# Optimization experiments

Measured on AMD Instinct MI355X. Metric: run time of the kernel, lower is better.

## Reference

```python
import jax, jax.numpy as jnp
import numpy as np

K = 512  # number of activations kept per row (init_kwargs k)


def setup_inputs() -> dict:
    key = jax.random.key(0)
    x = jax.random.normal(key, (8192, 8192), dtype=jnp.float32)
    return {"x": x}


def reference(x):
    # torch.topk(x, k, dim=1) -> indices of k largest per row
    _, idx = jax.lax.top_k(x, K)                      # idx: [B, K]
    rows = jnp.arange(x.shape[0])[:, None]            # [B, 1]
    # zeros_like + scatter(1, idx, 1)
    mask = jnp.zeros_like(x).at[rows, idx].set(1.0)   # [B, F]
    return x * mask
```

## Files before the change

kernel.cpp:

```cpp
#include <hip/hip_runtime.h>
#include <stdint.h>

#define FDIM 8192
#define KSEL 512
#define NT   512
#define EPT  (FDIM / NT / 4)
#define NBIN 4096
#define NWAVE (NT / 64)

__device__ __forceinline__ unsigned keyOf(unsigned u) {
    return (u & 0x80000000u) ? ~u : (u | 0x80000000u);
}
__device__ __forceinline__ float valOf(unsigned key) {
    unsigned u = (key & 0x80000000u) ? (key ^ 0x80000000u) : ~key;
    return __uint_as_float(u);
}

__global__ __launch_bounds__(NT) void topk_mask_kernel(const float* __restrict__ x,
                                                       float* __restrict__ out) {
    __shared__ uint4 hist4[NBIN / 4];
    unsigned* hist = (unsigned*)hist4;
    __shared__ unsigned wtot[NWAVE];
    __shared__ unsigned s_prefix, s_need, s_sub, s_tiecnt;
    __shared__ unsigned tiebuf[64];

    const int row  = blockIdx.x;
    const int t    = threadIdx.x;
    const int lane = t & 63;
    const int wave = t >> 6;

    const float4* xrow = (const float4*)(x + (size_t)row * FDIM);
    float4*       orow = (float4*)(out + (size_t)row * FDIM);

    uint4 kreg[EPT];
    #pragma unroll
    for (int j = 0; j < EPT; ++j) {
        float4 v = xrow[j * NT + t];
        kreg[j].x = keyOf(__float_as_uint(v.x));
        kreg[j].y = keyOf(__float_as_uint(v.y));
        kreg[j].z = keyOf(__float_as_uint(v.z));
        kreg[j].w = keyOf(__float_as_uint(v.w));
    }
    #pragma unroll
    for (int i = t; i < NBIN / 4; i += NT) hist4[i] = make_uint4(0u, 0u, 0u, 0u);
    if (t == 0) { s_prefix = 0u; s_need = KSEL; s_tiecnt = 0u; }
    __syncthreads();

    #pragma unroll
    for (int round = 0; round < 3; ++round) {
        const unsigned pref = s_prefix;
        const unsigned need = s_need;

        if (round == 0) {
            #pragma unroll
            for (int j = 0; j < EPT; ++j) {
                #pragma unroll
                for (int c = 0; c < 4; ++c) {
                    unsigned key = (&kreg[j].x)[c];
                    atomicAdd(&hist[key >> 20], 1u);
                }
            }
        } else if (round == 1) {
            #pragma unroll
            for (int j = 0; j < EPT; ++j) {
                #pragma unroll
                for (int c = 0; c < 4; ++c) {
                    unsigned key = (&kreg[j].x)[c];
                    if ((key >> 20) == pref)
                        atomicAdd(&hist[(key >> 8) & 0xFFFu], 1u);
                }
            }
        } else {
            #pragma unroll
            for (int j = 0; j < EPT; ++j) {
                #pragma unroll
                for (int c = 0; c < 4; ++c) {
                    unsigned key = (&kreg[j].x)[c];
                    if ((key >> 8) == pref)
                        atomicAdd(&hist[key & 0xFFu], 1u);
                }
            }
        }
        __syncthreads();

        const unsigned b4 = (unsigned)t * 2u;
        const uint4 h0 = hist4[b4];
        const uint4 h1 = hist4[b4 + 1];
        unsigned sfx[9];
        sfx[8] = 0u;
        sfx[7] = h1.w;
        sfx[6] = sfx[7] + h1.z;
        sfx[5] = sfx[6] + h1.y;
        sfx[4] = sfx[5] + h1.x;
        sfx[3] = sfx[4] + h0.w;
        sfx[2] = sfx[3] + h0.z;
        sfx[1] = sfx[2] + h0.y;
        sfx[0] = sfx[1] + h0.x;
        hist4[b4]     = make_uint4(0u, 0u, 0u, 0u);
        hist4[b4 + 1] = make_uint4(0u, 0u, 0u, 0u);
        const unsigned tot = sfx[0];
        unsigned incl = tot;
        #pragma unroll
        for (int off = 1; off < 64; off <<= 1) {
            unsigned y = __shfl_down(incl, off);
            incl += (lane + off < 64) ? y : 0u;
        }
        if (lane == 0) wtot[wave] = incl;
        __syncthreads();
        unsigned gb = incl - tot;
        #pragma unroll
        for (int w = 0; w < NWAVE; ++w) gb += (w > wave) ? wtot[w] : 0u;

        const unsigned base = (unsigned)t * (NBIN / NT);
        #pragma unroll
        for (int i = 0; i < 8; ++i) {
            unsigned S = gb + sfx[i];
            unsigned h = sfx[i] - sfx[i + 1];
            if (S >= need && S - h < need) {
                s_prefix = (round == 2) ? ((pref << 8) | (base + (unsigned)i))
                                        : ((pref << 12) | (base + (unsigned)i));
                s_need = need - (S - h);
                s_sub  = h;
            }
        }
        __syncthreads();
    }

    const unsigned thresh = s_prefix;
    const unsigned keepEq = s_need;
    const unsigned eqCnt  = s_sub;
    const bool simple = (eqCnt == keepEq);

    if (simple) {
        #pragma unroll
        for (int j = 0; j < EPT; ++j) {
            uint4 k = kreg[j];
            float4 o;
            o.x = (k.x >= thresh) ? valOf(k.x) : 0.0f;
            o.y = (k.y >= thresh) ? valOf(k.y) : 0.0f;
            o.z = (k.z >= thresh) ? valOf(k.z) : 0.0f;
            o.w = (k.w >= thresh) ? valOf(k.w) : 0.0f;
            orow[j * NT + t] = o;
        }
    } else {
        #pragma unroll
        for (int j = 0; j < EPT; ++j) {
            uint4 k = kreg[j];
            float4 o;
            o.x = (k.x > thresh) ? valOf(k.x) : 0.0f;
            o.y = (k.y > thresh) ? valOf(k.y) : 0.0f;
            o.z = (k.z > thresh) ? valOf(k.z) : 0.0f;
            o.w = (k.w > thresh) ? valOf(k.w) : 0.0f;
            orow[j * NT + t] = o;
        }
        #pragma unroll
        for (int j = 0; j < EPT; ++j) {
            #pragma unroll
            for (int c = 0; c < 4; ++c) {
                unsigned key = (&kreg[j].x)[c];
                if (key == thresh) {
                    unsigned slot = atomicAdd(&s_tiecnt, 1u);
                    if (slot < 64u) tiebuf[slot] = 4u * (unsigned)(j * NT + t) + (unsigned)c;
                }
            }
        }
        __syncthreads();
        if (t == 0) {
            const unsigned m = s_tiecnt;
            const float v = valOf(thresh);
            if (m <= 64u) {
                for (unsigned i = 0; i < m; ++i) {
                    unsigned idx = tiebuf[i], rank = 0;
                    for (unsigned q = 0; q < m; ++q) rank += (tiebuf[q] < idx);
                    if (rank < keepEq) out[(size_t)row * FDIM + idx] = v;
                }
            } else {
                unsigned c = 0;
                for (int i = 0; i < FDIM && c < keepEq; ++i) {
                    if (keyOf(__float_as_uint(x[(size_t)row * FDIM + i])) == thresh) {
                        out[(size_t)row * FDIM + i] = v; ++c;
                    }
                }
            }
        }
    }
}

extern "C" void kernel_launch(void* const* d_in, const int* in_sizes, int n_in,
                              void* d_out, int out_size, void* d_ws, size_t ws_size,
                              hipStream_t stream) {
    const float* x = (const float*)d_in[0];
    float* out = (float*)d_out;
    topk_mask_kernel<<<dim3(FDIM), dim3(NT), 0, stream>>>(x, out);
}
```

Before: 439.2 us.

## Make kernel persistent over rows with register double-buffered prefetch of next row

Launches 1024 blocks that each process 8 rows, prefetching the next row's data into a second register buffer while the current row's radix-select runs, so global load latency overlaps the histogram work. Barriers are replaced with custom waitcnt and s_barrier sequences that wait only on LDS so the outstanding prefetch loads are not drained, and keyOf becomes branchless. This doubles the per-thread register footprint for row data, and launch_bounds(NT,4) may force spills or limit occupancy.

```diff
diff --git a/kernel.cpp b/kernel.cpp
--- a/kernel.cpp
+++ b/kernel.cpp
@@ -7,56 +7,70 @@
 #define EPT  (FDIM / NT / 4)
 #define NBIN 4096
 #define NWAVE (NT / 64)
+#define NBLK 1024
+#define RPB  (FDIM / NBLK)
 
 __device__ __forceinline__ unsigned keyOf(unsigned u) {
-    return (u & 0x80000000u) ? ~u : (u | 0x80000000u);
+    return u ^ ((unsigned)((int)u >> 31) | 0x80000000u);
 }
 __device__ __forceinline__ float valOf(unsigned key) {
     unsigned u = (key & 0x80000000u) ? (key ^ 0x80000000u) : ~key;
     return __uint_as_float(u);
 }
 
-__global__ __launch_bounds__(NT) void topk_mask_kernel(const float* __restrict__ x,
-                                                       float* __restrict__ out) {
-    __shared__ uint4 hist4[NBIN / 4];
-    unsigned* hist = (unsigned*)hist4;
-    __shared__ unsigned wtot[NWAVE];
-    __shared__ unsigned s_prefix, s_need, s_sub, s_tiecnt;
-    __shared__ unsigned tiebuf[64];
-
-    const int row  = blockIdx.x;
-    const int t    = threadIdx.x;
-    const int lane = t & 63;
-    const int wave = t >> 6;
-
-    const float4* xrow = (const float4*)(x + (size_t)row * FDIM);
-    float4*       orow = (float4*)(out + (size_t)row * FDIM);
-
-    uint4 kreg[EPT];
+__device__ __forceinline__ void barrier_lgkm() {
+    asm volatile("s_waitcnt lgkmcnt(0)" ::: "memory");
+    __builtin_amdgcn_s_barrier();
+}
+__device__ __forceinline__ void barrier_full() {
+    asm volatile("s_waitcnt vmcnt(0) lgkmcnt(0)" ::: "memory");
+    __builtin_amdgcn_s_barrier();
+}
+
+struct Shared {
+    uint4 hist4[NBIN / 4];
+    unsigned wtot[NWAVE];
+    unsigned s_prefix, s_need;
+    unsigned s_thresh, s_keepEq, s_eqCnt;
+    unsigned s_tiecnt;
+    unsigned tiebuf[64];
+};
+
+__device__ __forceinline__ void process_row(
+    const int row, const bool doPrefetch, const int nextRow,
+    const float* __restrict__ x, float* __restrict__ out,
+    uint4 (&cur)[EPT], uint4 (&nxt)[EPT],
+    Shared& sh, const int t, const int lane, const int wave)
+{
+    if (doPrefetch) {
+        const uint4* xr = (const uint4*)(x + (size_t)nextRow * FDIM);
+        #pragma unroll
+        for (int j = 0; j < EPT; ++j) nxt[j] = xr[j * NT + t];
+    }
+
     #pragma unroll
     for (int j = 0; j < EPT; ++j) {
-        float4 v = xrow[j * NT + t];
-        kreg[j].x = keyOf(__float_as_uint(v.x));
-        kreg[j].y = keyOf(__float_as_uint(v.y));
-        kreg[j].z = keyOf(__float_as_uint(v.z));
-        kreg[j].w = keyOf(__float_as_uint(v.w));
-    }
-    #pragma unroll
-    for (int i = t; i < NBIN / 4; i += NT) hist4[i] = make_uint4(0u, 0u, 0u, 0u);
-    if (t == 0) { s_prefix = 0u; s_need = KSEL; s_tiecnt = 0u; }
-    __syncthreads();
+        cur[j].x = keyOf(cur[j].x);
+        cur[j].y = keyOf(cur[j].y);
+        cur[j].z = keyOf(cur[j].z);
+        cur[j].w = keyOf(cur[j].w);
+    }
+    if (t == 0) { sh.s_prefix = 0u; sh.s_need = KSEL; sh.s_tiecnt = 0u; }
+    barrier_lgkm();
+
+    unsigned* hist = (unsigned*)sh.hist4;
 
     #pragma unroll
     for (int round = 0; round < 3; ++round) {
-        const unsigned pref = s_prefix;
-        const unsigned need = s_need;
+        const unsigned pref = sh.s_prefix;
+        const unsigned need = sh.s_need;
 
         if (round == 0) {
             #pragma unroll
             for (int j = 0; j < EPT; ++j) {
                 #pragma unroll
                 for (int c = 0; c < 4; ++c) {
-                    unsigned key = (&kreg[j].x)[c];
+                    unsigned key = (&cur[j].x)[c];
                     atomicAdd(&hist[key >> 20], 1u);
                 }
             }
@@ -65,7 +79,7 @@
             for (int j = 0; j < EPT; ++j) {
                 #pragma unroll
                 for (int c = 0; c < 4; ++c) {
-                    unsigned key = (&kreg[j].x)[c];
+                    unsigned key = (&cur[j].x)[c];
                     if ((key >> 20) == pref)
                         atomicAdd(&hist[(key >> 8) & 0xFFFu], 1u);
                 }
@@ -75,17 +89,17 @@
             for (int j = 0; j < EPT; ++j) {
                 #pragma unroll
                 for (int c = 0; c < 4; ++c) {
-                    unsigned key = (&kreg[j].x)[c];
+                    unsigned key = (&cur[j].x)[c];
                     if ((key >> 8) == pref)
                         atomicAdd(&hist[key & 0xFFu], 1u);
                 }
             }
         }
-        __syncthreads();
+        barrier_lgkm();
 
         const unsigned b4 = (unsigned)t * 2u;
-        const uint4 h0 = hist4[b4];
-        const uint4 h1 = hist4[b4 + 1];
+        const uint4 h0 = sh.hist4[b4];
+        const uint4 h1 = sh.hist4[b4 + 1];
         unsigned sfx[9];
         sfx[8] = 0u;
         sfx[7] = h1.w;
@@ -96,8 +110,8 @@
         sfx[2] = sfx[3] + h0.z;
         sfx[1] = sfx[2] + h0.y;
         sfx[0] = sfx[1] + h0.x;
-        hist4[b4]     = make_uint4(0u, 0u, 0u, 0u);
-        hist4[b4 + 1] = make_uint4(0u, 0u, 0u, 0u);
+        sh.hist4[b4]     = make_uint4(0u, 0u, 0u, 0u);
+        sh.hist4[b4 + 1] = make_uint4(0u, 0u, 0u, 0u);
         const unsigned tot = sfx[0];
         unsigned incl = tot;
         #pragma unroll
@@ -105,11 +119,12 @@
             unsigned y = __shfl_down(incl, off);
             incl += (lane + off < 64) ? y : 0u;
         }
-        if (lane == 0) wtot[wave] = incl;
-        __syncthreads();
+        if (lane == 0) sh.wtot[wave] = incl;
+        barrier_lgkm();
+
         unsigned gb = incl - tot;
         #pragma unroll
-        for (int w = 0; w < NWAVE; ++w) gb += (w > wave) ? wtot[w] : 0u;
+        for (int w = 0; w < NWAVE; ++w) gb += (w > wave) ? sh.wtot[w] : 0u;
 
         const unsigned base = (unsigned)t * (NBIN / NT);
         #pragma unroll
@@ -117,24 +132,30 @@
             unsigned S = gb + sfx[i];
             unsigned h = sfx[i] - sfx[i + 1];
             if (S >= need && S - h < need) {
-                s_prefix = (round == 2) ? ((pref << 8) | (base + (unsigned)i))
-                                        : ((pref << 12) | (base + (unsigned)i));
-                s_need = need - (S - h);
-                s_sub  = h;
-            }
-        }
-        __syncthreads();
-    }
-
-    const unsigned thresh = s_prefix;
-    const unsigned keepEq = s_need;
-    const unsigned eqCnt  = s_sub;
+                if (round == 2) {
+                    sh.s_thresh = (pref << 8) | (base + (unsigned)i);
+                    sh.s_keepEq = need - (S - h);
+                    sh.s_eqCnt  = h;
+                } else {
+                    sh.s_prefix = (pref << 12) | (base + (unsigned)i);
+                    sh.s_need   = need - (S - h);
+                }
+            }
+        }
+        barrier_lgkm();
+    }
+
+    const unsigned thresh = sh.s_thresh;
+    const unsigned keepEq = sh.s_keepEq;
+    const unsigned eqCnt  = sh.s_eqCnt;
     const bool simple = (eqCnt == keepEq);
 
+    float4* orow = (float4*)(out + (size_t)row * FDIM);
+
     if (simple) {
         #pragma unroll
         for (int j = 0; j < EPT; ++j) {
-            uint4 k = kreg[j];
+            uint4 k = cur[j];
             float4 o;
             o.x = (k.x >= thresh) ? valOf(k.x) : 0.0f;
             o.y = (k.y >= thresh) ? valOf(k.y) : 0.0f;
@@ -145,7 +166,7 @@
     } else {
         #pragma unroll
         for (int j = 0; j < EPT; ++j) {
-            uint4 k = kreg[j];
+            uint4 k = cur[j];
             float4 o;
             o.x = (k.x > thresh) ? valOf(k.x) : 0.0f;
             o.y = (k.y > thresh) ? valOf(k.y) : 0.0f;
@@ -157,21 +178,21 @@
         for (int j = 0; j < EPT; ++j) {
             #pragma unroll
             for (int c = 0; c < 4; ++c) {
-                unsigned key = (&kreg[j].x)[c];
+                unsigned key = (&cur[j].x)[c];
                 if (key == thresh) {
-                    unsigned slot = atomicAdd(&s_tiecnt, 1u);
-                    if (slot < 64u) tiebuf[slot] = 4u * (unsigned)(j * NT + t) + (unsigned)c;
-                }
-            }
-        }
-        __syncthreads();
+                    unsigned slot = atomicAdd(&sh.s_tiecnt, 1u);
+                    if (slot < 64u) sh.tiebuf[slot] = 4u * (unsigned)(j * NT + t) + (unsigned)c;
+                }
+            }
+        }
+        barrier_full();
         if (t == 0) {
-            const unsigned m = s_tiecnt;
+            const unsigned m = sh.s_tiecnt;
             const float v = valOf(thresh);
             if (m <= 64u) {
                 for (unsigned i = 0; i < m; ++i) {
-                    unsigned idx = tiebuf[i], rank = 0;
-                    for (unsigned q = 0; q < m; ++q) rank += (tiebuf[q] < idx);
+                    unsigned idx = sh.tiebuf[i], rank = 0;
+                    for (unsigned q = 0; q < m; ++q) rank += (sh.tiebuf[q] < idx);
                     if (rank < keepEq) out[(size_t)row * FDIM + idx] = v;
                 }
             } else {
@@ -186,10 +207,37 @@
     }
 }
 
+__global__ __launch_bounds__(NT, 4) void topk_mask_kernel(const float* __restrict__ x,
+                                                          float* __restrict__ out) {
+    __shared__ Shared sh;
+
+    const int blk  = blockIdx.x;
+    const int t    = threadIdx.x;
+    const int lane = t & 63;
+    const int wave = t >> 6;
+
+    uint4 rawA[EPT], rawB[EPT];
+    {
+        const uint4* xr = (const uint4*)(x + (size_t)blk * FDIM);
+        #pragma unroll
+        for (int j = 0; j < EPT; ++j) rawA[j] = xr[j * NT + t];
+    }
+    #pragma unroll
+    for (int i = t; i < NBIN / 4; i += NT) sh.hist4[i] = make_uint4(0u, 0u, 0u, 0u);
+
+    #pragma unroll 1
+    for (int r = 0; r < RPB; r += 2) {
+        process_row(r * NBLK + blk, true, (r + 1) * NBLK + blk,
+                    x, out, rawA, rawB, sh, t, lane, wave);
+        process_row((r + 1) * NBLK + blk, (r + 2) < RPB, (r + 2) * NBLK + blk,
+                    x, out, rawB, rawA, sh, t, lane, wave);
+    }
+}
+
 extern "C" void kernel_launch(void* const* d_in, const int* in_sizes, int n_in,
                               void* d_out, int out_size, void* d_ws, size_t ws_size,
                               hipStream_t stream) {
     const float* x = (const float*)d_in[0];
     float* out = (float*)d_out;
-    topk_mask_kernel<<<dim3(FDIM), dim3(NT), 0, stream>>>(x, out);
-}
+    topk_mask_kernel<<<dim3(NBLK), dim3(NT), 0, stream>>>(x, out);
+}
```

Result: no change. 444.8 us (+1.3%).
